# Kernel tuning notes

Measured on AMD Instinct MI355X. Metric: run time of the kernel, lower is better.

## Reference

```python
import jax, jax.numpy as jnp
import numpy as np
from jax import lax

N_NODES = 16384
N_EDGES = 262144
T = 64
F_IN = 8
H1, C1 = 12, 16          # globals H and O in the source
HID2 = H1 * C1           # 192, input to second GATConv
LSTM_H = 128
TRAIN_LEN = 32
TARGET_ID = 0
NEG_SLOPE = 0.2


def setup_inputs() -> dict:
    key = jax.random.key(0)
    ks = jax.random.split(key, 16)
    x = jax.random.normal(ks[0], (T, N_NODES, F_IN), jnp.float32)
    src = jax.random.randint(ks[1], (T, N_EDGES), 0, N_NODES)
    dst = jax.random.randint(ks[2], (T, N_EDGES), 0, N_NODES)
    dst = jnp.where(dst == src, (dst + 1) % N_NODES, dst)  # guarantee no self-loops
    edge_index = jnp.stack([src, dst], axis=1)  # (T, 2, E)
    g = lambda k, sh: jax.random.normal(k, sh, jnp.float32) * 0.1
    return {
        "x": x, "edge_index": edge_index,
        "Wl1": g(ks[3], (F_IN, H1 * C1)),
        "att_l1": g(ks[4], (1, H1, C1)), "att_r1": g(ks[5], (1, H1, C1)),
        "b1": jnp.zeros((H1 * C1,), jnp.float32),
        "Wl2": g(ks[6], (HID2, 1)),
        "att_l2": g(ks[7], (1, 1, 1)), "att_r2": g(ks[8], (1, 1, 1)),
        "b2": jnp.zeros((1,), jnp.float32),
        "Wih0": g(ks[9], (4 * LSTM_H, 1)), "Whh0": g(ks[10], (4 * LSTM_H, LSTM_H)),
        "bih0": jnp.zeros((4 * LSTM_H,), jnp.float32), "bhh0": jnp.zeros((4 * LSTM_H,), jnp.float32),
        "Wih1": g(ks[11], (4 * LSTM_H, LSTM_H)), "Whh1": g(ks[12], (4 * LSTM_H, LSTM_H)),
        "bih1": jnp.zeros((4 * LSTM_H,), jnp.float32), "bhh1": jnp.zeros((4 * LSTM_H,), jnp.float32),
        "Wlin": g(ks[13], (1, LSTM_H)), "blin": jnp.zeros((1,), jnp.float32),
    }


def _gat(x, ei, W, att_l, att_r, b, heads, outc, concat):
    N = x.shape[0]
    xl = (x @ W).reshape(N, heads, outc)              # (N,H,C)
    al = jnp.sum(xl * att_l, axis=-1)                 # (N,H)
    ar = jnp.sum(xl * att_r, axis=-1)                 # (N,H)
    loop = jnp.arange(N)
    src = jnp.concatenate([ei[0], loop])              # add self loops (inputs have none)
    dst = jnp.concatenate([ei[1], loop])
    alpha = jax.nn.leaky_relu(al[src] + ar[dst], NEG_SLOPE)  # (E+N, H)
    # segment softmax over destination neighborhoods
    amax = jax.ops.segment_max(alpha, dst, num_segments=N)
    ex = jnp.exp(alpha - amax[dst])
    alpha = ex / (jax.ops.segment_sum(ex, dst, num_segments=N)[dst] + 1e-16)
    # hardcoded per-edge-row edits from message(): s and v copies, then blend
    s = alpha.at[jnp.array([1, 2, 12, 19, 22])].set(0.0).at[jnp.array([7, 14])].set(1.0)
    v = alpha.at[jnp.array([10, 13])].set(0.5).at[jnp.array([17])].set(0.0)
    alpha = 0.8 * alpha + 0.1 * s + 0.1 * v
    out = jax.ops.segment_sum(xl[src] * alpha[:, :, None], dst, num_segments=N)  # (N,H,C)
    out = out.reshape(N, heads * outc) if concat else out.mean(axis=1)
    return out + b


def _lstm_layer(xs, Wih, Whh, bih, bhh):
    # xs: (L, B, in) -> hs: (L, B, H); torch gate order i,f,g,o
    Bsz, Hd = xs.shape[1], Whh.shape[1]
    def step(carry, xt):
        h, c = carry
        gates = xt @ Wih.T + h @ Whh.T + bih + bhh
        i, f, g, o = jnp.split(gates, 4, axis=-1)
        c = jax.nn.sigmoid(f) * c + jax.nn.sigmoid(i) * jnp.tanh(g)
        h = jax.nn.sigmoid(o) * jnp.tanh(c)
        return (h, c), h
    init = (jnp.zeros((Bsz, Hd), xs.dtype), jnp.zeros((Bsz, Hd), xs.dtype))
    _, hs = lax.scan(step, init, xs)
    return hs


def reference(x, edge_index, Wl1, att_l1, att_r1, b1, Wl2, att_l2, att_r2, b2,
              Wih0, Whh0, bih0, bhh0, Wih1, Whh1, bih1, bhh1, Wlin, blin):
    def per_t(args):
        xt, eit = args
        h = _gat(xt, eit, Wl1, att_l1, att_r1, b1, H1, C1, True)
        h = jax.nn.elu(h)
        h = _gat(h, eit, Wl2, att_l2, att_r2, b2, 1, 1, False)
        return h[:, 0]
    out = lax.map(per_t, (x, edge_index))             # (T, N) == xs_out
    series = lax.stop_gradient(out[:, TARGET_ID])     # split_sequences detaches
    idx = jnp.arange(T - TRAIN_LEN)[:, None] + jnp.arange(TRAIN_LEN)[None, :]
    ts = series[idx][:, :, None]                      # (B, L, 1), batch_first
    xs = jnp.transpose(ts, (1, 0, 2))                 # (L, B, 1)
    hs = _lstm_layer(xs, Wih0, Whh0, bih0, bhh0)
    hs = _lstm_layer(hs, Wih1, Whh1, bih1, bhh1)
    return hs[-1] @ Wlin.T + blin                     # (B, 1)
```

## Files before the change

kernel.cpp:

```cpp
#include <hip/hip_runtime.h>
#include <math.h>

#define T 64
#define NN 16384
#define NE 262144
#define FIN 8
#define H1H 12
#define C1C 16
#define HID 192
#define CAP2 95
#define SCAP 96
#define DEGCAP 127
#define LH 128
#define G4 512
#define NB 32
#define NL 32

#define DEV __device__ __forceinline__

DEV float wave_max(float v){
  #pragma unroll
  for (int m = 32; m; m >>= 1) v = fmaxf(v, __shfl_xor(v, m));
  return v;
}
DEV float wave_sum(float v){
  #pragma unroll
  for (int m = 32; m; m >>= 1) v += __shfl_xor(v, m);
  return v;
}
DEV float leaky(float x){ return x >= 0.f ? x : 0.2f * x; }
DEV float sigmoidf(float x){ return 1.f / (1.f + expf(-x)); }

DEV float apply_edit(float a, int eid){
  if (eid >= 32) return a;
  const unsigned m09 = (1u<<1)|(1u<<2)|(1u<<7)|(1u<<10)|(1u<<12)|(1u<<13)|(1u<<14)|(1u<<17)|(1u<<19)|(1u<<22);
  const unsigned mp1 = (1u<<7)|(1u<<14);
  const unsigned mp05 = (1u<<10)|(1u<<13);
  unsigned b = 1u << eid;
  float r = (m09 & b) ? 0.9f * a : a;
  if (mp1 & b) r += 0.1f;
  if (mp05 & b) r += 0.05f;
  return r;
}

__global__ __launch_bounds__(256) void k_scan0(const int* __restrict__ ei,
                                               int* __restrict__ cnt2, int* __restrict__ list2){
  long long gid = (long long)blockIdx.x * blockDim.x + threadIdx.x;
  long long e4 = gid * 4;
  int t = (int)(e4 >> 18);
  int e = (int)(e4 & (NE - 1));
  const int* dstp = ei + (size_t)t * 2 * NE + NE + e;
  int4 d = *(const int4*)dstp;
  int dd[4] = {d.x, d.y, d.z, d.w};
  #pragma unroll
  for (int q = 0; q < 4; q++){
    if (dd[q] == 0){
      int pos = atomicAdd(&cnt2[t], 1);
      if (pos < CAP2) list2[t * CAP2 + pos] = e + q;
    }
  }
}

__global__ __launch_bounds__(128) void k_build(const int* __restrict__ ei, const int* __restrict__ cnt2,
                                               const int* __restrict__ list2, int* __restrict__ scnt,
                                               int* __restrict__ Slist, int* __restrict__ slot_of){
  int t = blockIdx.x;
  int* so = slot_of + (size_t)t * NN;
  int m = min(cnt2[t], CAP2);
  for (int i = threadIdx.x; i < m + 1; i += blockDim.x){
    int u = (i == m) ? 0 : ei[(size_t)t * 2 * NE + list2[t * CAP2 + i]];
    int old = atomicCAS(&so[u], -1, -2);
    if (old == -1){
      int s = atomicAdd(&scnt[t], 1);
      Slist[t * SCAP + s] = u;
      __hip_atomic_store(&so[u], s, __ATOMIC_RELAXED, __HIP_MEMORY_SCOPE_AGENT);
    }
  }
}

__global__ __launch_bounds__(256) void k_scan1(const int* __restrict__ ei, const int* __restrict__ slot_of,
                                               int* __restrict__ ecnt1, int* __restrict__ elist1){
  long long gid = (long long)blockIdx.x * blockDim.x + threadIdx.x;
  long long e4 = gid * 4;
  int t = (int)(e4 >> 18);
  int e = (int)(e4 & (NE - 1));
  const int* dstp = ei + (size_t)t * 2 * NE + NE + e;
  int4 d = *(const int4*)dstp;
  int dd[4] = {d.x, d.y, d.z, d.w};
  #pragma unroll
  for (int q = 0; q < 4; q++){
    int sl = slot_of[(size_t)t * NN + dd[q]];
    if (sl >= 0){
      int pos = atomicAdd(&ecnt1[t * SCAP + sl], 1);
      if (pos < DEGCAP) elist1[((size_t)t * SCAP + sl) * DEGCAP + pos] = e + q;
    }
  }
}

__global__ __launch_bounds__(64, 4) void k_gat1(const float* __restrict__ x, const int* __restrict__ ei,
                                             const float* __restrict__ Wl1, const float* __restrict__ attl,
                                             const float* __restrict__ attr, const float* __restrict__ b1,
                                             const int* __restrict__ scnt, const int* __restrict__ Slist,
                                             const int* __restrict__ ecnt1, const int* __restrict__ elist1,
                                             float* __restrict__ h1){
  int t = blockIdx.y, s = blockIdx.x, h = blockIdx.z;
  if (s >= scnt[t]) return;
  int lane = threadIdx.x;
  int u = Slist[t * SCAP + s];
  int deg = min(ecnt1[t * SCAP + s], DEGCAP);
  int tot = deg + 1;
  bool two = tot > 64;
  const float* xt = x + (size_t)t * NN * FIN;
  const int* srcp = ei + (size_t)t * 2 * NE;
  const int* el = elist1 + ((size_t)t * SCAP + s) * DEGCAP;

  float4 xu_a = ((const float4*)(xt + (size_t)u * FIN))[0];
  float4 xu_b = ((const float4*)(xt + (size_t)u * FIN))[1];
  float xu[FIN] = {xu_a.x, xu_a.y, xu_a.z, xu_a.w, xu_b.x, xu_b.y, xu_b.z, xu_b.w};

  bool act0 = lane < tot;
  int eid0 = 1 << 29;
  int su0 = u;
  if (lane < deg){ int e = el[lane]; eid0 = e; su0 = srcp[e]; }
  float4 xs0a = ((const float4*)(xt + (size_t)su0 * FIN))[0];
  float4 xs0b = ((const float4*)(xt + (size_t)su0 * FIN))[1];
  float xsrc0[FIN] = {xs0a.x, xs0a.y, xs0a.z, xs0a.w, xs0b.x, xs0b.y, xs0b.z, xs0b.w};

  bool act1 = false; int eid1 = 1 << 29;
  float xsrc1[FIN];
  if (two){
    int idx = 64 + lane;
    act1 = idx < tot;
    int su1 = u;
    if (idx < deg){ int e = el[idx]; eid1 = e; su1 = srcp[e]; }
    float4 xs1a = ((const float4*)(xt + (size_t)su1 * FIN))[0];
    float4 xs1b = ((const float4*)(xt + (size_t)su1 * FIN))[1];
    #pragma unroll
    for (int f = 0; f < 4; f++) xsrc1[f] = (&xs1a.x)[f];
    #pragma unroll
    for (int f = 0; f < 4; f++) xsrc1[4 + f] = (&xs1b.x)[f];
  }

  const float* Wh = Wl1 + h * C1C;
  const float* attlh = attl + h * C1C;
  const float* attrh = attr + h * C1C;

  float ar = 0.f;
  #pragma unroll
  for (int c = 0; c < C1C; c++){
    float v = 0.f;
    #pragma unroll
    for (int f = 0; f < FIN; f++) v = fmaf(xu[f], Wh[f * HID + c], v);
    ar = fmaf(v, attrh[c], ar);
  }

  float xls0[C1C];
  float al0 = 0.f;
  #pragma unroll
  for (int c = 0; c < C1C; c++){
    float v = 0.f;
    #pragma unroll
    for (int f = 0; f < FIN; f++) v = fmaf(xsrc0[f], Wh[f * HID + c], v);
    xls0[c] = v;
    al0 = fmaf(v, attlh[c], al0);
  }
  float raw0 = act0 ? leaky(al0 + ar) : -INFINITY;

  float xls1[C1C];
  float raw1 = -INFINITY;
  if (two){
    float al1 = 0.f;
    #pragma unroll
    for (int c = 0; c < C1C; c++){
      float v = 0.f;
      #pragma unroll
      for (int f = 0; f < FIN; f++) v = fmaf(xsrc1[f], Wh[f * HID + c], v);
      xls1[c] = v;
      al1 = fmaf(v, attlh[c], al1);
    }
    raw1 = act1 ? leaky(al1 + ar) : -INFINITY;
  }

  float M = wave_max(fmaxf(raw0, raw1));
  float ex0 = act0 ? expf(raw0 - M) : 0.f;
  float ex1 = act1 ? expf(raw1 - M) : 0.f;
  float S = wave_sum(ex0 + ex1);
  float den = S + 1e-16f;
  float alpha0 = apply_edit(ex0 / den, eid0);
  float alpha1 = two ? apply_edit(ex1 / den, eid1) : 0.f;

  float sum[C1C];
  #pragma unroll
  for (int c = 0; c < C1C; c++){
    sum[c] = xls0[c] * alpha0;
    if (two) sum[c] = fmaf(xls1[c], alpha1, sum[c]);
  }
  #pragma unroll
  for (int m = 32; m; m >>= 1){
    #pragma unroll
    for (int c = 0; c < C1C; c++) sum[c] += __shfl_xor(sum[c], m);
  }
  if (lane == 0){
    float* h1p = h1 + ((size_t)t * SCAP + s) * HID + h * C1C;
    #pragma unroll
    for (int c = 0; c < C1C; c++){
      float v = sum[c] + b1[h * C1C + c];
      h1p[c] = v > 0.f ? v : expm1f(v);
    }
  }
}

__global__ __launch_bounds__(64) void k_gat2(const int* __restrict__ ei, const float* __restrict__ Wl2,
                                             const float* __restrict__ attl2_, const float* __restrict__ attr2_,
                                             const float* __restrict__ b2, const int* __restrict__ cnt2,
                                             const int* __restrict__ list2, const int* __restrict__ slot_of,
                                             const float* __restrict__ h1, float* __restrict__ series){
  int t = blockIdx.x; int lane = threadIdx.x;
  int deg = min(cnt2[t], CAP2);
  int tot = deg + 1;
  const int* srcp = ei + (size_t)t * 2 * NE;
  const int* so = slot_of + (size_t)t * NN;
  float attl2 = attl2_[0], attr2 = attr2_[0];
  int sl0 = so[0];
  const float* h1t = h1 + (size_t)t * SCAP * HID;

  float x0 = 0.f;
  for (int k = 0; k < HID; k++) x0 += h1t[(size_t)sl0 * HID + k] * Wl2[k];

  bool act[2]; int eid[2]; float xl2[2];
  #pragma unroll
  for (int ch = 0; ch < 2; ch++){
    int idx = ch * 64 + lane;
    act[ch] = idx < tot;
    eid[ch] = 1 << 29;
    int sl = sl0;
    if (idx < deg){ int e = list2[t * CAP2 + idx]; eid[ch] = e; sl = so[srcp[e]]; }
    float v = 0.f;
    if (act[ch]) for (int k = 0; k < HID; k++) v += h1t[(size_t)sl * HID + k] * Wl2[k];
    xl2[ch] = v;
  }
  float raw[2];
  #pragma unroll
  for (int ch = 0; ch < 2; ch++) raw[ch] = act[ch] ? leaky(attl2 * xl2[ch] + attr2 * x0) : -INFINITY;
  float M = wave_max(fmaxf(raw[0], raw[1]));
  float ex[2];
  #pragma unroll
  for (int ch = 0; ch < 2; ch++) ex[ch] = act[ch] ? expf(raw[ch] - M) : 0.f;
  float S = wave_sum(ex[0] + ex[1]);
  float den = S + 1e-16f;
  float contrib = apply_edit(ex[0] / den, eid[0]) * xl2[0] + apply_edit(ex[1] / den, eid[1]) * xl2[1];
  contrib = wave_sum(contrib);
  if (lane == 0) series[t] = contrib + b2[0];
}

#define AT_LOADR(p)    __hip_atomic_load((p), __ATOMIC_RELAXED, __HIP_MEMORY_SCOPE_AGENT)
#define AT_STORER(p,v) __hip_atomic_store((p), (v), __ATOMIC_RELAXED, __HIP_MEMORY_SCOPE_AGENT)

#define REP32(M) M(0)M(1)M(2)M(3)M(4)M(5)M(6)M(7)M(8)M(9)M(10)M(11)M(12)M(13)M(14)M(15)\
                 M(16)M(17)M(18)M(19)M(20)M(21)M(22)M(23)M(24)M(25)M(26)M(27)M(28)M(29)M(30)M(31)
#define WDECL(i) float4 w##i;
#define WLOAD(i) w##i = Wr[i];
#define WPIN(i)  asm volatile("" : "+v"(w##i.x), "+v"(w##i.y), "+v"(w##i.z), "+v"(w##i.w));
#define WFMA(i)  { float4 hv = h4[i]; a0 = fmaf(w##i.x, hv.x, a0); a1 = fmaf(w##i.y, hv.y, a1); \
                   a2 = fmaf(w##i.z, hv.z, a2); a3 = fmaf(w##i.w, hv.w, a3); }

__global__ __launch_bounds__(512, 2) void k_lstm(const float* __restrict__ series,
    const float* __restrict__ Wih0, const float* __restrict__ Whh0,
    const float* __restrict__ bih0, const float* __restrict__ bhh0,
    const float* __restrict__ Wih1, const float* __restrict__ Whh1,
    const float* __restrict__ bih1, const float* __restrict__ bhh1,
    const float* __restrict__ Wlin, const float* __restrict__ blin,
    float* __restrict__ h0g, float* __restrict__ xpart,
    int* __restrict__ flagA, int* __restrict__ flagB, float* __restrict__ out){
  int j = threadIdx.x;
  int st = blockIdx.x >> 5;
  int b = blockIdx.x & 31;
  __shared__ __align__(16) float h_lds[LH];
  __shared__ __align__(16) float c_lds[LH];
  __shared__ float gate_lds[G4];
  __shared__ float s_series[NL];
  __shared__ int rdy_lds;
  const float4* h4 = (const float4*)h_lds;

  if (st == 0){
    const float4* Wr = (const float4*)(Whh0 + (size_t)j * LH);
    REP32(WDECL)
    REP32(WLOAD)
    REP32(WPIN)
    float wih = Wih0[j];
    float bsum = bih0[j] + bhh0[j];
    if (j < LH){ h_lds[j] = 0.f; c_lds[j] = 0.f; }
    if (j < NL) s_series[j] = series[b + j];
    __syncthreads();
    for (int t = 0; t < NL; t++){
      float a0 = 0.f, a1 = 0.f, a2 = 0.f, a3 = 0.f;
      REP32(WFMA)
      float acc = fmaf(wih, s_series[t], bsum) + (a0 + a1) + (a2 + a3);
      gate_lds[j] = acc;
      __syncthreads();
      if (j < LH){
        float ig = sigmoidf(gate_lds[j]);
        float fg = sigmoidf(gate_lds[LH + j]);
        float gg = tanhf(gate_lds[2 * LH + j]);
        float og = sigmoidf(gate_lds[3 * LH + j]);
        float c = fg * c_lds[j] + ig * gg;
        float h = og * tanhf(c);
        c_lds[j] = c; h_lds[j] = h;
        AT_STORER(&h0g[(b * NL + t) * LH + j], h);
      }
      __syncthreads();
      if (j == 0) AT_STORER(&flagA[b], t + 1);
    }
  } else if (st == 1){
    const float4* Wr = (const float4*)(Wih1 + (size_t)j * LH);
    REP32(WDECL)
    REP32(WLOAD)
    REP32(WPIN)
    int ready = 0;
    for (int t = 0; t < NL; t++){
      if (ready <= t){
        if (j == 0){
          int f;
          while ((f = AT_LOADR(&flagA[b])) < t + 1) __builtin_amdgcn_s_sleep(1);
          rdy_lds = f;
        }
        __syncthreads();
        ready = rdy_lds;
      }
      if (j < LH) h_lds[j] = AT_LOADR(&h0g[(b * NL + t) * LH + j]);
      __syncthreads();
      float a0 = 0.f, a1 = 0.f, a2 = 0.f, a3 = 0.f;
      REP32(WFMA)
      AT_STORER(&xpart[(b * NL + t) * G4 + j], (a0 + a1) + (a2 + a3));
      __syncthreads();
      if (j == 0) AT_STORER(&flagB[b], t + 1);
    }
  } else {
    const float4* Wr = (const float4*)(Whh1 + (size_t)j * LH);
    REP32(WDECL)
    REP32(WLOAD)
    REP32(WPIN)
    float bsum = bih1[j] + bhh1[j];
    if (j < LH){ h_lds[j] = 0.f; c_lds[j] = 0.f; }
    __syncthreads();
    int ready = 0;
    for (int t = 0; t < NL; t++){
      if (ready <= t){
        if (j == 0){
          int f;
          while ((f = AT_LOADR(&flagB[b])) < t + 1) __builtin_amdgcn_s_sleep(1);
          rdy_lds = f;
        }
        __syncthreads();
        ready = rdy_lds;
      }
      float xj = AT_LOADR(&xpart[(b * NL + t) * G4 + j]);
      float a0 = 0.f, a1 = 0.f, a2 = 0.f, a3 = 0.f;
      REP32(WFMA)
      float acc = xj + bsum + (a0 + a1) + (a2 + a3);
      gate_lds[j] = acc;
      __syncthreads();
      if (j < LH){
        float ig = sigmoidf(gate_lds[j]);
        float fg = sigmoidf(gate_lds[LH + j]);
        float gg = tanhf(gate_lds[2 * LH + j]);
        float og = sigmoidf(gate_lds[3 * LH + j]);
        float c = fg * c_lds[j] + ig * gg;
        float h = og * tanhf(c);
        c_lds[j] = c; h_lds[j] = h;
      }
      __syncthreads();
    }
    if (j == 0){
      float s2 = blin[0];
      for (int k = 0; k < LH; k++) s2 += Wlin[k] * h_lds[k];
      out[b] = s2;
    }
  }
}

extern "C" void kernel_launch(void* const* d_in, const int* in_sizes, int n_in,
                              void* d_out, int out_size, void* d_ws, size_t ws_size,
                              hipStream_t stream) {
  const float* x     = (const float*)d_in[0];
  const int*   ei    = (const int*)  d_in[1];
  const float* Wl1   = (const float*)d_in[2];
  const float* attl1 = (const float*)d_in[3];
  const float* attr1 = (const float*)d_in[4];
  const float* b1    = (const float*)d_in[5];
  const float* Wl2   = (const float*)d_in[6];
  const float* attl2 = (const float*)d_in[7];
  const float* attr2 = (const float*)d_in[8];
  const float* b2    = (const float*)d_in[9];
  const float* Wih0  = (const float*)d_in[10];
  const float* Whh0  = (const float*)d_in[11];
  const float* bih0  = (const float*)d_in[12];
  const float* bhh0  = (const float*)d_in[13];
  const float* Wih1  = (const float*)d_in[14];
  const float* Whh1  = (const float*)d_in[15];
  const float* bih1  = (const float*)d_in[16];
  const float* bhh1  = (const float*)d_in[17];
  const float* Wlin  = (const float*)d_in[18];
  const float* blin  = (const float*)d_in[19];
  float* out = (float*)d_out;

  char* wsb = (char*)d_ws;
  size_t off = 0;
  auto alloc = [&](size_t bytes)->void*{
    void* p = wsb + off;
    off += (bytes + 255) & ~(size_t)255;
    return p;
  };
  int* cnt2  = (int*)alloc(T * 4);
  int* scnt  = (int*)alloc(T * 4);
  int* ecnt1 = (int*)alloc(T * SCAP * 4);
  int* flagA = (int*)alloc(NB * 4);
  int* flagB = (int*)alloc(NB * 4);
  size_t ctrl_bytes = off;
  int* slot_of = (int*)alloc((size_t)T * NN * 4);
  int* list2   = (int*)alloc((size_t)T * CAP2 * 4);
  int* Slist   = (int*)alloc((size_t)T * SCAP * 4);
  int* elist1  = (int*)alloc((size_t)T * SCAP * DEGCAP * 4);
  float* h1    = (float*)alloc((size_t)T * SCAP * HID * 4);
  float* series= (float*)alloc(T * 4);
  float* h0g   = (float*)alloc((size_t)NB * NL * LH * 4);
  float* xpart = (float*)alloc((size_t)NB * NL * G4 * 4);

  hipMemsetAsync(d_ws, 0, ctrl_bytes, stream);
  hipMemsetAsync(slot_of, 0xFF, (size_t)T * NN * 4, stream);

  k_scan0<<<T * NE / 4 / 256, 256, 0, stream>>>(ei, cnt2, list2);
  k_build<<<T, 128, 0, stream>>>(ei, cnt2, list2, scnt, Slist, slot_of);
  k_scan1<<<T * NE / 4 / 256, 256, 0, stream>>>(ei, slot_of, ecnt1, elist1);
  k_gat1<<<dim3(SCAP, T, H1H), 64, 0, stream>>>(x, ei, Wl1, attl1, attr1, b1, scnt, Slist, ecnt1, elist1, h1);
  k_gat2<<<T, 64, 0, stream>>>(ei, Wl2, attl2, attr2, b2, cnt2, list2, slot_of, h1, series);
  k_lstm<<<96, 512, 0, stream>>>(series, Wih0, Whh0, bih0, bhh0, Wih1, Whh1, bih1, bhh1,
                                 Wlin, blin, h0g, xpart, flagA, flagB, out);
}
```

Before: 419.2 us.

## Run LSTM layers sequentially in one block per batch, removing cross-block flag pipeline

Replaces the three-stage producer/consumer pipeline across 96 blocks (layer0 recurrence, layer1 input projection, layer1 recurrence, synchronised through global flags and spin-waits) with 32 blocks. Each block runs the three phases one after another and keeps the intermediate h0 and input projections in LDS. Gate nonlinearities are now applied by all 512 threads before the barrier instead of by 128 threads after it. This removes global-memory flag polling and the atomic traffic, but gives up overlap between layers, so the critical path becomes the sum of the phases. It also uses about 82KB of LDS per block.

```diff
diff --git a/kernel.cpp b/kernel.cpp
--- a/kernel.cpp
+++ b/kernel.cpp
@@ -253,15 +253,12 @@
   if (lane == 0) series[t] = contrib + b2[0];
 }
 
-#define AT_LOADR(p)    __hip_atomic_load((p), __ATOMIC_RELAXED, __HIP_MEMORY_SCOPE_AGENT)
-#define AT_STORER(p,v) __hip_atomic_store((p), (v), __ATOMIC_RELAXED, __HIP_MEMORY_SCOPE_AGENT)
-
 #define REP32(M) M(0)M(1)M(2)M(3)M(4)M(5)M(6)M(7)M(8)M(9)M(10)M(11)M(12)M(13)M(14)M(15)\
                  M(16)M(17)M(18)M(19)M(20)M(21)M(22)M(23)M(24)M(25)M(26)M(27)M(28)M(29)M(30)M(31)
 #define WDECL(i) float4 w##i;
 #define WLOAD(i) w##i = Wr[i];
 #define WPIN(i)  asm volatile("" : "+v"(w##i.x), "+v"(w##i.y), "+v"(w##i.z), "+v"(w##i.w));
-#define WFMA(i)  { float4 hv = h4[i]; a0 = fmaf(w##i.x, hv.x, a0); a1 = fmaf(w##i.y, hv.y, a1); \
+#define WFMA(i)  { float4 hv = hp[i]; a0 = fmaf(w##i.x, hv.x, a0); a1 = fmaf(w##i.y, hv.y, a1); \
                    a2 = fmaf(w##i.z, hv.z, a2); a3 = fmaf(w##i.w, hv.w, a3); }
 
 __global__ __launch_bounds__(512, 2) void k_lstm(const float* __restrict__ series,
@@ -270,20 +267,21 @@
     const float* __restrict__ Wih1, const float* __restrict__ Whh1,
     const float* __restrict__ bih1, const float* __restrict__ bhh1,
     const float* __restrict__ Wlin, const float* __restrict__ blin,
-    float* __restrict__ h0g, float* __restrict__ xpart,
-    int* __restrict__ flagA, int* __restrict__ flagB, float* __restrict__ out){
+    float* __restrict__ out){
   int j = threadIdx.x;
-  int st = blockIdx.x >> 5;
-  int b = blockIdx.x & 31;
+  int b = blockIdx.x;
   __shared__ __align__(16) float h_lds[LH];
   __shared__ __align__(16) float c_lds[LH];
-  __shared__ float gate_lds[G4];
-  __shared__ float s_series[NL];
-  __shared__ int rdy_lds;
-  const float4* h4 = (const float4*)h_lds;
-
-  if (st == 0){
+  __shared__ __align__(16) float gate_lds[G4];
+  __shared__ __align__(16) float s_series[NL];
+  __shared__ __align__(16) float h0buf[NL][LH];
+  __shared__ __align__(16) float xp_lds[NL * G4];
+
+  int cls = j >> 7;
+
+  {
     const float4* Wr = (const float4*)(Whh0 + (size_t)j * LH);
+    const float4* hp = (const float4*)h_lds;
     REP32(WDECL)
     REP32(WLOAD)
     REP32(WPIN)
@@ -296,77 +294,50 @@
       float a0 = 0.f, a1 = 0.f, a2 = 0.f, a3 = 0.f;
       REP32(WFMA)
       float acc = fmaf(wih, s_series[t], bsum) + (a0 + a1) + (a2 + a3);
-      gate_lds[j] = acc;
+      gate_lds[j] = (cls == 2) ? tanhf(acc) : sigmoidf(acc);
       __syncthreads();
       if (j < LH){
-        float ig = sigmoidf(gate_lds[j]);
-        float fg = sigmoidf(gate_lds[LH + j]);
-        float gg = tanhf(gate_lds[2 * LH + j]);
-        float og = sigmoidf(gate_lds[3 * LH + j]);
-        float c = fg * c_lds[j] + ig * gg;
-        float h = og * tanhf(c);
-        c_lds[j] = c; h_lds[j] = h;
-        AT_STORER(&h0g[(b * NL + t) * LH + j], h);
+        float c = gate_lds[LH + j] * c_lds[j] + gate_lds[j] * gate_lds[2 * LH + j];
+        float h = gate_lds[3 * LH + j] * tanhf(c);
+        c_lds[j] = c; h_lds[j] = h; h0buf[t][j] = h;
       }
       __syncthreads();
-      if (j == 0) AT_STORER(&flagA[b], t + 1);
-    }
-  } else if (st == 1){
+    }
+  }
+
+  {
     const float4* Wr = (const float4*)(Wih1 + (size_t)j * LH);
     REP32(WDECL)
     REP32(WLOAD)
     REP32(WPIN)
-    int ready = 0;
     for (int t = 0; t < NL; t++){
-      if (ready <= t){
-        if (j == 0){
-          int f;
-          while ((f = AT_LOADR(&flagA[b])) < t + 1) __builtin_amdgcn_s_sleep(1);
-          rdy_lds = f;
-        }
-        __syncthreads();
-        ready = rdy_lds;
-      }
-      if (j < LH) h_lds[j] = AT_LOADR(&h0g[(b * NL + t) * LH + j]);
-      __syncthreads();
+      const float4* hp = (const float4*)h0buf[t];
       float a0 = 0.f, a1 = 0.f, a2 = 0.f, a3 = 0.f;
       REP32(WFMA)
-      AT_STORER(&xpart[(b * NL + t) * G4 + j], (a0 + a1) + (a2 + a3));
-      __syncthreads();
-      if (j == 0) AT_STORER(&flagB[b], t + 1);
-    }
-  } else {
+      xp_lds[t * G4 + j] = (a0 + a1) + (a2 + a3);
+    }
+  }
+
+  {
     const float4* Wr = (const float4*)(Whh1 + (size_t)j * LH);
+    const float4* hp = (const float4*)h_lds;
     REP32(WDECL)
     REP32(WLOAD)
     REP32(WPIN)
     float bsum = bih1[j] + bhh1[j];
+    __syncthreads();
     if (j < LH){ h_lds[j] = 0.f; c_lds[j] = 0.f; }
     __syncthreads();
-    int ready = 0;
     for (int t = 0; t < NL; t++){
-      if (ready <= t){
-        if (j == 0){
-          int f;
-          while ((f = AT_LOADR(&flagB[b])) < t + 1) __builtin_amdgcn_s_sleep(1);
-          rdy_lds = f;
-        }
-        __syncthreads();
-        ready = rdy_lds;
-      }
-      float xj = AT_LOADR(&xpart[(b * NL + t) * G4 + j]);
+      float xj = xp_lds[t * G4 + j];
       float a0 = 0.f, a1 = 0.f, a2 = 0.f, a3 = 0.f;
       REP32(WFMA)
       float acc = xj + bsum + (a0 + a1) + (a2 + a3);
-      gate_lds[j] = acc;
+      gate_lds[j] = (cls == 2) ? tanhf(acc) : sigmoidf(acc);
       __syncthreads();
       if (j < LH){
-        float ig = sigmoidf(gate_lds[j]);
-        float fg = sigmoidf(gate_lds[LH + j]);
-        float gg = tanhf(gate_lds[2 * LH + j]);
-        float og = sigmoidf(gate_lds[3 * LH + j]);
-        float c = fg * c_lds[j] + ig * gg;
-        float h = og * tanhf(c);
+        float c = gate_lds[LH + j] * c_lds[j] + gate_lds[j] * gate_lds[2 * LH + j];
+        float h = gate_lds[3 * LH + j] * tanhf(c);
         c_lds[j] = c; h_lds[j] = h;
       }
       __syncthreads();
@@ -414,8 +385,6 @@
   int* cnt2  = (int*)alloc(T * 4);
   int* scnt  = (int*)alloc(T * 4);
   int* ecnt1 = (int*)alloc(T * SCAP * 4);
-  int* flagA = (int*)alloc(NB * 4);
-  int* flagB = (int*)alloc(NB * 4);
   size_t ctrl_bytes = off;
   int* slot_of = (int*)alloc((size_t)T * NN * 4);
   int* list2   = (int*)alloc((size_t)T * CAP2 * 4);
@@ -423,8 +392,6 @@
   int* elist1  = (int*)alloc((size_t)T * SCAP * DEGCAP * 4);
   float* h1    = (float*)alloc((size_t)T * SCAP * HID * 4);
   float* series= (float*)alloc(T * 4);
-  float* h0g   = (float*)alloc((size_t)NB * NL * LH * 4);
-  float* xpart = (float*)alloc((size_t)NB * NL * G4 * 4);
 
   hipMemsetAsync(d_ws, 0, ctrl_bytes, stream);
   hipMemsetAsync(slot_of, 0xFF, (size_t)T * NN * 4, stream);
@@ -434,6 +401,6 @@
   k_scan1<<<T * NE / 4 / 256, 256, 0, stream>>>(ei, slot_of, ecnt1, elist1);
   k_gat1<<<dim3(SCAP, T, H1H), 64, 0, stream>>>(x, ei, Wl1, attl1, attr1, b1, scnt, Slist, ecnt1, elist1, h1);
   k_gat2<<<T, 64, 0, stream>>>(ei, Wl2, attl2, attr2, b2, cnt2, list2, slot_of, h1, series);
-  k_lstm<<<96, 512, 0, stream>>>(series, Wih0, Whh0, bih0, bhh0, Wih1, Whh1, bih1, bhh1,
-                                 Wlin, blin, h0g, xpart, flagA, flagB, out);
-}
+  k_lstm<<<NB, 512, 0, stream>>>(series, Wih0, Whh0, bih0, bhh0, Wih1, Whh1, bih1, bhh1,
+                                 Wlin, blin, out);
+}
```

Result: slower. 483.8 us (+15.4%).
